# Kernel tuning notes

Measured on AMD Instinct MI355X. Metric: run time of the kernel, lower is better.

The kernel has to match this reference:

```python
import jax, jax.numpy as jnp
import numpy as np

HEADS = 8

def _conv(x, w, b, stride, pad):
    # x: [B,C,H,W], w: [O,I,kh,kw] (torch OIHW layout)
    y = jax.lax.conv_general_dilated(x, w, (stride, stride), ((pad, pad), (pad, pad)),
                                     dimension_numbers=('NCHW', 'OIHW', 'NCHW'))
    return y + b[None, :, None, None]

def _maxpool2x2(x):
    # returns pooled values and one-hot argmax per 2x2 window (torch first-max tie-break)
    b, c, H, W = x.shape
    win = x.reshape(b, c, H // 2, 2, W // 2, 2).transpose(0, 1, 2, 4, 3, 5).reshape(b, c, H // 2, W // 2, 4)
    am = jnp.argmax(win, axis=-1)
    oh = jax.nn.one_hot(am, 4, dtype=x.dtype)
    pooled = jnp.sum(win * oh, axis=-1)
    return pooled, oh

def _maxunpool2x2(y, oh):
    b, c, h2, w2 = y.shape
    out = y[..., None] * oh  # [b,c,h2,w2,4]
    out = out.reshape(b, c, h2, w2, 2, 2).transpose(0, 1, 2, 4, 3, 5).reshape(b, c, h2 * 2, w2 * 2)
    return out

def _mha2d(x, wq, wk, wv, wo):
    # x: [b,c,h,w]; wq/wk/wv/wo stored as [in,out] so y = x @ W
    b, c, h, w = x.shape
    hw = h * w
    dk = wq.shape[1]
    dh = dk // HEADS
    xt = x.reshape(b, c, hw).transpose(0, 2, 1)  # [b,hw,c]
    def split(y):  # torch: view(b,hw,dh,heads).permute(0,3,1,2)
        return y.reshape(b, hw, dh, HEADS).transpose(0, 3, 1, 2)  # [b,heads,hw,dh]
    q = split(xt @ wq)
    k = split(xt @ wk)
    v = split(xt @ wv)
    scale = jnp.sqrt(jnp.asarray(dh, x.dtype))
    attn = jax.nn.softmax(jnp.einsum('bhqd,bhkd->bhqk', q, k) / scale, axis=-1)
    o = jnp.einsum('bhqk,bhkd->bhqd', attn, v)
    o = o.transpose(0, 2, 3, 1).reshape(b, hw, dk)  # [b,hw,dh,heads] -> merge
    o = o @ wo
    return o.transpose(0, 2, 1).reshape(b, dk, h, w)

def setup_inputs() -> dict:
    key = jax.random.key(0)
    ks = jax.random.split(key, 10)
    B, C, H, W = 16, 256, 64, 64
    s = 0.05
    return {
        'x': jax.random.normal(ks[0], (B, C, H, W), jnp.float32),
        'conv_w': jax.random.normal(ks[1], (C, C, 3, 3), jnp.float32) * s,
        'conv_b': jax.random.normal(ks[2], (C,), jnp.float32) * s,
        'fr_w': jax.random.normal(ks[3], (C, C, 1, 1), jnp.float32) * s,
        'fr_b': jax.random.normal(ks[4], (C,), jnp.float32) * s,
        'wq': jax.random.normal(ks[5], (C, C), jnp.float32) * s,
        'wk': jax.random.normal(ks[6], (C, C), jnp.float32) * s,
        'wv': jax.random.normal(ks[7], (C, C), jnp.float32) * s,
        'wo': jax.random.normal(ks[8], (C, C), jnp.float32) * s,
        'gamma': jax.random.normal(ks[9], (1,), jnp.float32) * 0.1,
    }

def reference(x, conv_w, conv_b, fr_w, fr_b, wq, wk, wv, wo, gamma):
    _x = _conv(x, fr_w, fr_b, 1, 0)          # 1x1 feature reduction
    _x, oh = _maxpool2x2(_x)                 # MaxPool2d(2, return_indices=True)
    _x = _mha2d(_x, wq, wk, wv, wo)          # attention over pooled grid
    _x = _maxunpool2x2(_x, oh)               # MaxUnpool2d(2)
    return _x * jnp.tanh(gamma[0]) + _conv(x, conv_w, conv_b, 1, 1)
```

## Files before the change

### kernel.cpp

```cpp
#include <hip/hip_runtime.h>
#include <hip/hip_bf16.h>
#include <math.h>

#define B 16
#define C 256
#define H 64
#define W 64
#define H2 32
#define W2 32
#define HW2 1024
#define HEADS 8
#define DH 32

typedef unsigned short ushort_t;
using short8 = __attribute__((ext_vector_type(8))) short;
using u16x8  = __attribute__((ext_vector_type(8))) unsigned short;
using f32x4  = __attribute__((ext_vector_type(4))) float;

__device__ inline ushort_t f2bf(float f) {
    __hip_bfloat16 hb = __float2bfloat16(f);
    return *(ushort_t*)&hb;
}
__device__ inline float bf2f(ushort_t u) {
    return __uint_as_float(((unsigned)u) << 16);
}

__device__ __forceinline__ void cp16(const ushort_t* g, ushort_t* l) {
    __builtin_amdgcn_global_load_lds(
        (const __attribute__((address_space(1))) void*)g,
        (__attribute__((address_space(3))) void*)l, 16, 0, 0);
}

#define RSCALE 0.17677669529663687f

__global__ __launch_bounds__(256) void k_prep_wT(const float* __restrict__ cw,
                                                 ushort_t* __restrict__ wbfT) {
    int i = threadIdx.x, o = blockIdx.x;
    const float* src = cw + ((size_t)o * C + i) * 9;
#pragma unroll
    for (int kk = 0; kk < 9; kk++)
        wbfT[((size_t)kk * C + o) * C + i] = f2bf(src[kk]);
}

__global__ __launch_bounds__(256) void k_prep_wx(
    const float* __restrict__ wq, const float* __restrict__ wk,
    const float* __restrict__ wv, const float* __restrict__ wo,
    const float* __restrict__ frw, ushort_t* __restrict__ wqkvT,
    ushort_t* __restrict__ woT, ushort_t* __restrict__ wfr) {
    int op = blockIdx.x, mat = blockIdx.y, t = threadIdx.x;
    if (mat < 3) {
        const float* w = (mat == 0) ? wq : (mat == 1) ? wk : wv;
        int hh = op >> 5, d = op & 31, col = d * 8 + hh;
        wqkvT[(size_t)mat * 65536 + op * 256 + t] = f2bf(w[t * 256 + col]);
    } else if (mat == 3) {
        int hh = t >> 5, d = t & 31, ic = d * 8 + hh;
        woT[op * 256 + t] = f2bf(wo[ic * 256 + op]);
    } else {
        wfr[op * 256 + t] = f2bf(frw[op * 256 + t]);
    }
}

__global__ __launch_bounds__(256) void k_prep_xn(const float* __restrict__ x,
                                                 ushort_t* __restrict__ xn) {
    __shared__ ushort_t ldsT[64 * 258];
    int t = threadIdx.x;
    int hp = blockIdx.x, b = blockIdx.y;
    ushort_t* dst = xn + ((size_t)(b * 66 + hp)) * 66 * 256;

    if (hp == 0 || hp == 65) {
        u16x8 z = (u16x8){0, 0, 0, 0, 0, 0, 0, 0};
        for (int i = t; i < 2112; i += 256) *(u16x8*)(dst + i * 8) = z;
        return;
    }
    const float* xb = x + ((size_t)b * 256) * 4096 + (size_t)(hp - 1) * 64;
    {
        int cq = t >> 6, w = t & 63;
#pragma unroll 8
        for (int it = 0; it < 64; ++it) {
            int c = it * 4 + cq;
            float v = xb[(size_t)c * 4096 + w];
            ldsT[w * 258 + c] = f2bf(v);
        }
    }
    __syncthreads();
    {
        u16x8 z = (u16x8){0, 0, 0, 0, 0, 0, 0, 0};
        if (t < 32) *(u16x8*)(dst + t * 8) = z;
        else if (t < 64) *(u16x8*)(dst + 65 * 256 + (t - 32) * 8) = z;
    }
    {
        int half = t >> 7, cl = t & 127;
#pragma unroll 4
        for (int it = 0; it < 32; ++it) {
            int w = it * 2 + half;
            unsigned v = *(const unsigned*)&ldsT[w * 258 + cl * 2];
            *(unsigned*)(dst + (size_t)(w + 1) * 256 + cl * 2) = v;
        }
    }
}

__global__ __launch_bounds__(256) void k_conv1pool_mfma(
    const ushort_t* __restrict__ xn, const ushort_t* __restrict__ wfr,
    const float* __restrict__ frb, ushort_t* __restrict__ Pbf,
    unsigned char* __restrict__ idx) {
    __shared__ __align__(16) ushort_t sh[32768];
    ushort_t* Als = sh;
    ushort_t* Bls = sh + 8192;
    int t = threadIdx.x;
    int wg = blockIdx.x;
    int mt = (wg & 7) * 64 + (wg >> 3);
    int b = mt >> 5;
    int h0 = (mt * 2) & 63;

    int r = t >> 2, p = t & 3;
    int kswz = (p ^ ((r >> 1) & 3)) * 8;
    const ushort_t* aB0 = xn + ((size_t)((b * 66 + h0 + 1) * 66 + (r + 1))) * 256 + kswz;
    const ushort_t* aB1 = xn + ((size_t)((b * 66 + h0 + 2) * 66 + (r + 1))) * 256 + kswz;
    const ushort_t* bB = wfr + (size_t)r * 256 + kswz;

    f32x4 acc[4][8];
#pragma unroll
    for (int mf = 0; mf < 4; mf++)
#pragma unroll
        for (int nf = 0; nf < 8; nf++) acc[mf][nf] = (f32x4){0.f, 0.f, 0.f, 0.f};

    cp16(aB0, &Als[t * 8]);
    cp16(aB1, &Als[2048 + t * 8]);
    cp16(bB, &Bls[t * 8]);
    cp16(bB + 64 * 256, &Bls[2048 + t * 8]);
    cp16(bB + 128 * 256, &Bls[4096 + t * 8]);
    cp16(bB + 192 * 256, &Bls[6144 + t * 8]);
    __syncthreads();

    int l = t & 63, wid = t >> 6, wm = wid >> 1, wn = wid & 1;
    int arow = wm * 64 + (l & 15);
    int brow = wn * 128 + (l & 15);
    int pslot = ((l >> 4) ^ ((l >> 1) & 3)) * 8;

    for (int s = 0; s < 8; s++) {
        int cur = s & 1;
        if (s < 7) {
            int off = (s + 1) * 32;
            int nb = cur ^ 1;
            cp16(aB0 + off, &Als[nb * 4096 + t * 8]);
            cp16(aB1 + off, &Als[nb * 4096 + 2048 + t * 8]);
            cp16(bB + off, &Bls[nb * 8192 + t * 8]);
            cp16(bB + 64 * 256 + off, &Bls[nb * 8192 + 2048 + t * 8]);
            cp16(bB + 128 * 256 + off, &Bls[nb * 8192 + 4096 + t * 8]);
            cp16(bB + 192 * 256 + off, &Bls[nb * 8192 + 6144 + t * 8]);
        }
        short8 af[4], bf[8];
#pragma unroll
        for (int mf = 0; mf < 4; mf++)
            af[mf] = *(const short8*)&Als[cur * 4096 + (arow + mf * 16) * 32 + pslot];
#pragma unroll
        for (int nf = 0; nf < 8; nf++)
            bf[nf] = *(const short8*)&Bls[cur * 8192 + (brow + nf * 16) * 32 + pslot];
#pragma unroll
        for (int mf = 0; mf < 4; mf++)
#pragma unroll
            for (int nf = 0; nf < 8; nf++)
                acc[mf][nf] = __builtin_amdgcn_mfma_f32_16x16x32_bf16(
                    af[mf], bf[nf], acc[mf][nf], 0, 0, 0);
        __syncthreads();
    }

#pragma unroll
    for (int nf = 0; nf < 8; nf++) {
        int o = wn * 128 + nf * 16 + (l & 15);
        float bias = frb[o];
#pragma unroll
        for (int mf = 0; mf < 4; mf++) {
            int rbase = wm * 64 + mf * 16 + ((l >> 4) << 2);
            f32x4 a = acc[mf][nf];
#pragma unroll
            for (int jj = 0; jj < 4; jj++)
                sh[(rbase + jj) * 256 + o] = f2bf(a[jj] + bias);
        }
    }
    __syncthreads();

    {
        int h2 = mt & 31;
        size_t rowb = (size_t)(b << 10) + h2 * 32;
        int o0 = (t & 31) * 8;
#pragma unroll
        for (int pp = 0; pp < 4; pp++) {
            int w2 = pp * 8 + (t >> 5);
            u16x8 r0 = *(const u16x8*)&sh[(2 * w2) * 256 + o0];
            u16x8 r1 = *(const u16x8*)&sh[(2 * w2 + 1) * 256 + o0];
            u16x8 r2 = *(const u16x8*)&sh[(64 + 2 * w2) * 256 + o0];
            u16x8 r3 = *(const u16x8*)&sh[(64 + 2 * w2 + 1) * 256 + o0];
            u16x8 pv;
            unsigned amlo = 0, amhi = 0;
#pragma unroll
            for (int e = 0; e < 8; e++) {
                float v0 = bf2f(r0[e]), v1 = bf2f(r1[e]);
                float v2 = bf2f(r2[e]), v3 = bf2f(r3[e]);
                float m = v0;
                ushort_t raw = r0[e];
                unsigned am = 0;
                if (v1 > m) { m = v1; raw = r1[e]; am = 1; }
                if (v2 > m) { m = v2; raw = r2[e]; am = 2; }
                if (v3 > m) { m = v3; raw = r3[e]; am = 3; }
                pv[e] = raw;
                if (e < 4) amlo |= am << (8 * e);
                else       amhi |= am << (8 * (e - 4));
            }
            size_t po = (rowb + w2) * 256 + o0;
            *(u16x8*)(Pbf + po) = pv;
            *(uint2*)(idx + po) = make_uint2(amlo, amhi);
        }
    }
}

__global__ __launch_bounds__(256) void k_qkv_mfma(
    const ushort_t* __restrict__ A, const ushort_t* __restrict__ Bw,
    ushort_t* __restrict__ qb, ushort_t* __restrict__ kb,
    ushort_t* __restrict__ vtb) {
    __shared__ __align__(16) ushort_t Als[2][4096];
    __shared__ __align__(16) ushort_t Bls[2][4096];
    int t = threadIdx.x;
    int wg = blockIdx.x;
    int linear = (wg & 7) * 96 + (wg >> 3);
    int mt = linear / 6, nt = linear % 6;

    int r = t >> 2, p = t & 3;
    int kswz = (p ^ ((r >> 1) & 3)) * 8;
    const ushort_t* aB0 = A + ((size_t)(mt * 128 + r)) * 256 + kswz;
    const ushort_t* aB1 = aB0 + (size_t)64 * 256;
    const ushort_t* bB0 = Bw + ((size_t)(nt * 128 + r)) * 256 + kswz;
    const ushort_t* bB1 = bB0 + (size_t)64 * 256;

    f32x4 acc[4][4];
#pragma unroll
    for (int mf = 0; mf < 4; mf++)
#pragma unroll
        for (int nf = 0; nf < 4; nf++) acc[mf][nf] = (f32x4){0.f, 0.f, 0.f, 0.f};

    cp16(aB0, &Als[0][t * 8]);
    cp16(aB1, &Als[0][2048 + t * 8]);
    cp16(bB0, &Bls[0][t * 8]);
    cp16(bB1, &Bls[0][2048 + t * 8]);
    __syncthreads();

    int l = t & 63, wid = t >> 6, wm = wid >> 1, wn = wid & 1;
    int arow = wm * 64 + (l & 15);
    int brow = wn * 64 + (l & 15);
    int pslot = ((l >> 4) ^ ((l >> 1) & 3)) * 8;

    for (int s = 0; s < 8; s++) {
        int cur = s & 1;
        if (s < 7) {
            int off = (s + 1) * 32;
            int nb = cur ^ 1;
            cp16(aB0 + off, &Als[nb][t * 8]);
            cp16(aB1 + off, &Als[nb][2048 + t * 8]);
            cp16(bB0 + off, &Bls[nb][t * 8]);
            cp16(bB1 + off, &Bls[nb][2048 + t * 8]);
        }
        short8 af[4], bf[4];
#pragma unroll
        for (int mf = 0; mf < 4; mf++)
            af[mf] = *(const short8*)&Als[cur][(arow + mf * 16) * 32 + pslot];
#pragma unroll
        for (int nf = 0; nf < 4; nf++)
            bf[nf] = *(const short8*)&Bls[cur][(brow + nf * 16) * 32 + pslot];
#pragma unroll
        for (int mf = 0; mf < 4; mf++)
#pragma unroll
            for (int nf = 0; nf < 4; nf++)
                acc[mf][nf] = __builtin_amdgcn_mfma_f32_16x16x32_bf16(
                    af[mf], bf[nf], acc[mf][nf], 0, 0, 0);
        __syncthreads();
    }

    if (nt < 4) {
        ushort_t* dst = (nt < 2) ? qb : kb;
        float sc = (nt < 2) ? RSCALE : 1.0f;
        int ccb = (nt & 1) * 128 + wn * 64;
#pragma unroll
        for (int nf = 0; nf < 4; nf++) {
            int cc = ccb + nf * 16 + (l & 15);
#pragma unroll
            for (int mf = 0; mf < 4; mf++) {
                int m = mt * 128 + wm * 64 + mf * 16 + ((l >> 4) << 2);
                f32x4 a = acc[mf][nf];
#pragma unroll
                for (int jj = 0; jj < 4; jj++)
                    dst[(size_t)(m + jj) * 256 + cc] = f2bf(a[jj] * sc);
            }
        }
    } else {
#pragma unroll
        for (int nf = 0; nf < 4; nf++) {
            int cc = (nt & 1) * 128 + wn * 64 + nf * 16 + (l & 15);
#pragma unroll
            for (int mf = 0; mf < 4; mf++) {
                int m = mt * 128 + wm * 64 + mf * 16 + ((l >> 4) << 2);
                int b = m >> 10, n0 = m & 1023;
                f32x4 a = acc[mf][nf];
                unsigned u0 = ((unsigned)f2bf(a[1]) << 16) | f2bf(a[0]);
                unsigned u1 = ((unsigned)f2bf(a[3]) << 16) | f2bf(a[2]);
                *(uint2*)&vtb[((size_t)(b * 256 + cc)) * 1024 + n0] =
                    make_uint2(u0, u1);
            }
        }
    }
}

__global__ __launch_bounds__(256) void k_attn_mfma(
    const ushort_t* __restrict__ qb, const ushort_t* __restrict__ kb,
    const ushort_t* __restrict__ vtb, ushort_t* __restrict__ aoT) {
    __shared__ __align__(16) ushort_t Klds[2][2048];
    __shared__ __align__(16) ushort_t Vlds[2][2048];
    __shared__ __align__(16) ushort_t Plds[4][2304];
    __shared__ float rs_lds[128];

    int t = threadIdx.x;
    int bid = blockIdx.x;
    int swz = (bid & 7) * 128 + (bid >> 3);
    int bh = swz >> 3, qt = swz & 7;
    int b = bh >> 3, h = bh & 7;
    int w = t >> 6, l = t & 63, g = l >> 4, li = l & 15;

    size_t qrow = (size_t)(b * 1024 + qt * 128 + w * 32 + li);
    short8 qv0 = *(const short8*)(qb + qrow * 256 + h * 32 + g * 8);
    short8 qv1 = *(const short8*)(qb + (qrow + 16) * 256 + h * 32 + g * 8);

    int sr = t >> 2, sp = t & 3;
    const ushort_t* kg =
        kb + ((size_t)(b * 1024 + sr)) * 256 + h * 32 + ((sp ^ ((sr >> 1) & 3)) * 8);
    int vd = t >> 3, vs = t & 7;
    const ushort_t* vg =
        vtb + ((size_t)(b * 256 + h * 32 + vd)) * 1024 + ((vs ^ (vd & 7)) * 8);

    f32x4 oacc[2][2];
    f32x4 rsv[2];
#pragma unroll
    for (int qf = 0; qf < 2; qf++) {
        rsv[qf] = (f32x4){0.f, 0.f, 0.f, 0.f};
#pragma unroll
        for (int df = 0; df < 2; df++) oacc[qf][df] = (f32x4){0.f, 0.f, 0.f, 0.f};
    }

    cp16(kg, &Klds[0][t * 8]);
    cp16(vg, &Vlds[0][t * 8]);
    __syncthreads();

    ushort_t* Pw = &Plds[w][0];

    for (int c = 0; c < 16; c++) {
        int cur = c & 1;
        if (c < 15) {
            cp16(kg + (size_t)(c + 1) * 64 * 256, &Klds[cur ^ 1][t * 8]);
            cp16(vg + (c + 1) * 64, &Vlds[cur ^ 1][t * 8]);
        }
        short8 ak[4];
#pragma unroll
        for (int kf = 0; kf < 4; kf++)
            ak[kf] = *(const short8*)&Klds[cur][(16 * kf + li) * 32 +
                                               ((g ^ ((l >> 1) & 3)) * 8)];
#pragma unroll
        for (int qf = 0; qf < 2; qf++) {
            short8 qv = qf ? qv1 : qv0;
#pragma unroll
            for (int kf = 0; kf < 4; kf++) {
                f32x4 st = __builtin_amdgcn_mfma_f32_16x16x32_bf16(
                    ak[kf], qv, (f32x4){0.f, 0.f, 0.f, 0.f}, 0, 0, 0);
                float p0 = __expf(st[0]), p1 = __expf(st[1]);
                float p2 = __expf(st[2]), p3 = __expf(st[3]);
                rsv[qf][0] += p0; rsv[qf][1] += p1;
                rsv[qf][2] += p2; rsv[qf][3] += p3;
                unsigned u0, u1;
                asm("v_cvt_pk_bf16_f32 %0, %1, %2" : "=v"(u0) : "v"(p0), "v"(p1));
                asm("v_cvt_pk_bf16_f32 %0, %1, %2" : "=v"(u1) : "v"(p2), "v"(p3));
                *(uint2*)&Pw[(16 * qf + li) * 72 + 16 * kf + 4 * g] =
                    make_uint2(u0, u1);
            }
        }
#pragma unroll
        for (int win = 0; win < 2; win++) {
            short8 pa[2], bv[2];
#pragma unroll
            for (int qf = 0; qf < 2; qf++)
                pa[qf] = *(const short8*)&Pw[(16 * qf + li) * 72 + win * 32 + 8 * g];
#pragma unroll
            for (int df = 0; df < 2; df++)
                bv[df] = *(const short8*)&Vlds[cur][(16 * df + li) * 64 +
                                                    (((win * 4 + g) ^ (l & 7)) * 8)];
#pragma unroll
            for (int qf = 0; qf < 2; qf++)
#pragma unroll
                for (int df = 0; df < 2; df++)
                    oacc[qf][df] = __builtin_amdgcn_mfma_f32_16x16x32_bf16(
                        pa[qf], bv[df], oacc[qf][df], 0, 0, 0);
        }
        __syncthreads();
    }

#pragma unroll
    for (int qf = 0; qf < 2; qf++) {
        float rs = (rsv[qf][0] + rsv[qf][1]) + (rsv[qf][2] + rsv[qf][3]);
        rs += __shfl_xor(rs, 16);
        rs += __shfl_xor(rs, 32);
        if (l < 16) rs_lds[w * 32 + 16 * qf + li] = rs;
    }
    __syncthreads();

#pragma unroll
    for (int qf = 0; qf < 2; qf++) {
        float4 rs4 = *(const float4*)&rs_lds[w * 32 + 16 * qf + 4 * g];
        float inv[4] = {1.f / rs4.x, 1.f / rs4.y, 1.f / rs4.z, 1.f / rs4.w};
#pragma unroll
        for (int df = 0; df < 2; df++) {
            f32x4 a = oacc[qf][df];
#pragma unroll
            for (int r2 = 0; r2 < 4; r2++) {
                size_t row = (size_t)(b * 1024 + qt * 128 + w * 32 + 16 * qf +
                                      4 * g + r2);
                aoT[row * 256 + h * 32 + 16 * df + li] = f2bf(a[r2] * inv[r2]);
            }
        }
    }
}

__global__ __launch_bounds__(256) void k_oproj_mfma(
    const ushort_t* __restrict__ A, const ushort_t* __restrict__ Bw,
    float* __restrict__ y2) {
    __shared__ __align__(16) ushort_t Als[2][4096];
    __shared__ __align__(16) ushort_t Bls[2][4096];
    int t = threadIdx.x;
    int wg = blockIdx.x;
    int linear = (wg & 7) * 32 + (wg >> 3);
    int nt = linear & 1, mt = linear >> 1;

    int r = t >> 2, p = t & 3;
    int kswz = (p ^ ((r >> 1) & 3)) * 8;
    const ushort_t* aB0 = A + ((size_t)(mt * 128 + r)) * 256 + kswz;
    const ushort_t* aB1 = aB0 + (size_t)64 * 256;
    const ushort_t* bB0 = Bw + ((size_t)(nt * 128 + r)) * 256 + kswz;
    const ushort_t* bB1 = bB0 + (size_t)64 * 256;

    f32x4 acc[4][4];
#pragma unroll
    for (int mf = 0; mf < 4; mf++)
#pragma unroll
        for (int nf = 0; nf < 4; nf++) acc[mf][nf] = (f32x4){0.f, 0.f, 0.f, 0.f};

    cp16(aB0, &Als[0][t * 8]);
    cp16(aB1, &Als[0][2048 + t * 8]);
    cp16(bB0, &Bls[0][t * 8]);
    cp16(bB1, &Bls[0][2048 + t * 8]);
    __syncthreads();

    int l = t & 63, wid = t >> 6, wm = wid >> 1, wn = wid & 1;
    int arow = wm * 64 + (l & 15);
    int brow = wn * 64 + (l & 15);
    int pslot = ((l >> 4) ^ ((l >> 1) & 3)) * 8;

    for (int s = 0; s < 8; s++) {
        int cur = s & 1;
        if (s < 7) {
            int off = (s + 1) * 32;
            int nb = cur ^ 1;
            cp16(aB0 + off, &Als[nb][t * 8]);
            cp16(aB1 + off, &Als[nb][2048 + t * 8]);
            cp16(bB0 + off, &Bls[nb][t * 8]);
            cp16(bB1 + off, &Bls[nb][2048 + t * 8]);
        }
        short8 af[4], bf[4];
#pragma unroll
        for (int mf = 0; mf < 4; mf++)
            af[mf] = *(const short8*)&Als[cur][(arow + mf * 16) * 32 + pslot];
#pragma unroll
        for (int nf = 0; nf < 4; nf++)
            bf[nf] = *(const short8*)&Bls[cur][(brow + nf * 16) * 32 + pslot];
#pragma unroll
        for (int mf = 0; mf < 4; mf++)
#pragma unroll
            for (int nf = 0; nf < 4; nf++)
                acc[mf][nf] = __builtin_amdgcn_mfma_f32_16x16x32_bf16(
                    af[mf], bf[nf], acc[mf][nf], 0, 0, 0);
        __syncthreads();
    }

#pragma unroll
    for (int nf = 0; nf < 4; nf++) {
        int cc = nt * 128 + wn * 64 + nf * 16 + (l & 15);
#pragma unroll
        for (int mf = 0; mf < 4; mf++) {
            int m = mt * 128 + wm * 64 + mf * 16 + ((l >> 4) << 2);
            f32x4 a = acc[mf][nf];
#pragma unroll
            for (int jj = 0; jj < 4; jj++)
                y2[(size_t)(m + jj) * 256 + cc] = a[jj];
        }
    }
}

__global__ __launch_bounds__(512) void k_conv3_mfma(
    const ushort_t* __restrict__ xn, const ushort_t* __restrict__ wbfT,
    const float* __restrict__ cb, const float* __restrict__ y2,
    const unsigned char* __restrict__ idx, const float* __restrict__ gamma,
    float* __restrict__ out) {
    extern __shared__ __align__(16) ushort_t lds[];
    ushort_t* AL = lds;
    ushort_t* BL = lds + 32768;
    int t = threadIdx.x;
    int mt = blockIdx.x;

    int srow = t >> 3, sslot = t & 7;
    int kel = (sslot ^ (srow & 7)) * 8;
    const ushort_t* aP[2][2];
    const ushort_t* bP[2][2];
#pragma unroll
    for (int hf = 0; hf < 2; hf++)
#pragma unroll
        for (int j = 0; j < 2; j++) {
            int row = hf * 128 + j * 64 + srow;
            int m = mt * 256 + row;
            int b0 = m >> 12, h0 = (m >> 6) & 63, w0 = m & 63;
            aP[hf][j] = xn + ((size_t)((b0 * 66 + h0) * 66 + w0)) * 256 + kel;
            bP[hf][j] = wbfT + (size_t)row * 256 + kel;
        }

    auto offA = [](int kt) -> int {
        int khkw = kt >> 2, it = kt & 3;
        int kh = khkw / 3, kw = khkw - kh * 3;
        return (kh * 66 + kw) * 256 + it * 64;
    };
    auto offB = [](int kt) -> int {
        return (kt >> 2) * 65536 + (kt & 3) * 64;
    };
    auto STAGE_A = [&](int bb, int hf, int kt) {
        int o = offA(kt);
        ushort_t* d = AL + bb * 16384 + hf * 8192 + t * 8;
        cp16(aP[hf][0] + o, d);
        cp16(aP[hf][1] + o, d + 4096);
    };
    auto STAGE_B = [&](int bb, int hf, int kt) {
        int o = offB(kt);
        ushort_t* d = BL + bb * 16384 + hf * 8192 + t * 8;
        cp16(bP[hf][0] + o, d);
        cp16(bP[hf][1] + o, d + 4096);
    };

    f32x4 acc[8][4];
#pragma unroll
    for (int mf = 0; mf < 8; mf++)
#pragma unroll
        for (int nf = 0; nf < 4; nf++) acc[mf][nf] = (f32x4){0.f, 0.f, 0.f, 0.f};

    STAGE_A(0, 0, 0); STAGE_A(0, 1, 0); STAGE_B(0, 0, 0); STAGE_B(0, 1, 0);
    STAGE_B(1, 0, 1); STAGE_A(1, 0, 1);
    asm volatile("s_waitcnt vmcnt(4)" ::: "memory");
    __builtin_amdgcn_s_barrier();
    __builtin_amdgcn_sched_barrier(0);

    int l = t & 63, wid = t >> 6, wm = wid >> 2, wn = wid & 3;
    int lr = l & 15, g = l >> 4, l7 = l & 7;
    int abase = wm * 8192;
    int bbase = (wn >> 1) * 8192 + (wn & 1) * 4096;

    for (int kt = 0; kt < 36; kt++) {
        int bb = kt & 1;
        const ushort_t* Ab = AL + bb * 16384 + abase;
        const ushort_t* Bb = BL + bb * 16384 + bbase;
        short8 afA[4][2], afB[4][2], bf0[2][2], bf1[2][2];
#pragma unroll
        for (int mf = 0; mf < 4; mf++)
#pragma unroll
            for (int kk = 0; kk < 2; kk++)
                afA[mf][kk] = *(const short8*)
                    &Ab[(mf * 16 + lr) * 64 + (((kk * 4 + g) ^ l7) * 8)];
#pragma unroll
        for (int nf = 0; nf < 2; nf++)
#pragma unroll
            for (int kk = 0; kk < 2; kk++)
                bf0[nf][kk] = *(const short8*)
                    &Bb[(nf * 16 + lr) * 64 + (((kk * 4 + g) ^ l7) * 8)];
        if (kt < 35) STAGE_A(bb ^ 1, 1, kt + 1);
        asm volatile("" ::: "memory");
        __builtin_amdgcn_s_barrier();
        __builtin_amdgcn_sched_barrier(0);
        __builtin_amdgcn_s_setprio(1);
#pragma unroll
        for (int kk = 0; kk < 2; kk++)
#pragma unroll
            for (int mf = 0; mf < 4; mf++)
#pragma unroll
                for (int nf = 0; nf < 2; nf++)
                    acc[mf][nf] = __builtin_amdgcn_mfma_f32_16x16x32_bf16(
                        afA[mf][kk], bf0[nf][kk], acc[mf][nf], 0, 0, 0);
        __builtin_amdgcn_s_setprio(0);
        asm volatile("" ::: "memory");
        __builtin_amdgcn_s_barrier();
        __builtin_amdgcn_sched_barrier(0);
#pragma unroll
        for (int nf = 0; nf < 2; nf++)
#pragma unroll
            for (int kk = 0; kk < 2; kk++)
                bf1[nf][kk] = *(const short8*)
                    &Bb[((nf + 2) * 16 + lr) * 64 + (((kk * 4 + g) ^ l7) * 8)];
        if (kt < 35) STAGE_B(bb ^ 1, 1, kt + 1);
        asm volatile("" ::: "memory");
        __builtin_amdgcn_s_barrier();
        __builtin_amdgcn_sched_barrier(0);
        __builtin_amdgcn_s_setprio(1);
#pragma unroll
        for (int kk = 0; kk < 2; kk++)
#pragma unroll
            for (int mf = 0; mf < 4; mf++)
#pragma unroll
                for (int nf = 0; nf < 2; nf++)
                    acc[mf][nf + 2] = __builtin_amdgcn_mfma_f32_16x16x32_bf16(
                        afA[mf][kk], bf1[nf][kk], acc[mf][nf + 2], 0, 0, 0);
        __builtin_amdgcn_s_setprio(0);
        asm volatile("" ::: "memory");
        __builtin_amdgcn_s_barrier();
        __builtin_amdgcn_sched_barrier(0);
#pragma unroll
        for (int mf = 0; mf < 4; mf++)
#pragma unroll
            for (int kk = 0; kk < 2; kk++)
                afB[mf][kk] = *(const short8*)
                    &Ab[((mf + 4) * 16 + lr) * 64 + (((kk * 4 + g) ^ l7) * 8)];
        if (kt < 34) STAGE_B(bb, 0, kt + 2);
        asm volatile("" ::: "memory");
        __builtin_amdgcn_s_barrier();
        __builtin_amdgcn_sched_barrier(0);
        __builtin_amdgcn_s_setprio(1);
#pragma unroll
        for (int kk = 0; kk < 2; kk++)
#pragma unroll
            for (int mf = 0; mf < 4; mf++)
#pragma unroll
                for (int nf = 0; nf < 2; nf++)
                    acc[mf + 4][nf] = __builtin_amdgcn_mfma_f32_16x16x32_bf16(
                        afB[mf][kk], bf0[nf][kk], acc[mf + 4][nf], 0, 0, 0);
        __builtin_amdgcn_s_setprio(0);
        asm volatile("" ::: "memory");
        __builtin_amdgcn_s_barrier();
        __builtin_amdgcn_sched_barrier(0);
        if (kt < 34) {
            STAGE_A(bb, 0, kt + 2);
            asm volatile("s_waitcnt vmcnt(4)" ::: "memory");
        } else {
            asm volatile("s_waitcnt vmcnt(0)" ::: "memory");
        }
        __builtin_amdgcn_s_barrier();
        __builtin_amdgcn_sched_barrier(0);
        __builtin_amdgcn_s_setprio(1);
#pragma unroll
        for (int kk = 0; kk < 2; kk++)
#pragma unroll
            for (int mf = 0; mf < 4; mf++)
#pragma unroll
                for (int nf = 0; nf < 2; nf++)
                    acc[mf + 4][nf + 2] = __builtin_amdgcn_mfma_f32_16x16x32_bf16(
                        afB[mf][kk], bf1[nf][kk], acc[mf + 4][nf + 2], 0, 0, 0);
        __builtin_amdgcn_s_setprio(0);
        asm volatile("" ::: "memory");
        __builtin_amdgcn_s_barrier();
        __builtin_amdgcn_sched_barrier(0);
    }

    float tg = tanhf(gamma[0]);
    int mbase = mt * 256 + wm * 128 + (g << 2);
    int obase = wn * 64 + lr;
#pragma unroll
    for (int nf = 0; nf < 4; nf++) {
        int o = obase + nf * 16;
        float bias = cb[o];
#pragma unroll
        for (int mf = 0; mf < 8; mf++) {
            int m = mbase + mf * 16;
            int b = m >> 12, h = (m >> 6) & 63, w0 = m & 63;
            const unsigned char* idr = idx + ((size_t)(b << 10)) * 256;
            const float* y2r = y2 + ((size_t)(b << 10)) * 256;
            f32x4 a = acc[mf][nf];
            float v4[4];
#pragma unroll
            for (int jj = 0; jj < 4; jj++) {
                int wj = w0 + jj;
                int n2 = ((h >> 1) << 5) + (wj >> 1);
                int j2 = ((h & 1) << 1) + (wj & 1);
                float val = a[jj] + bias;
                if (idr[(size_t)n2 * 256 + o] == (unsigned char)j2)
                    val += tg * y2r[(size_t)n2 * 256 + o];
                v4[jj] = val;
            }
            *(float4*)(out + (((size_t)(b * C + o) * H + h) << 6) + w0) =
                make_float4(v4[0], v4[1], v4[2], v4[3]);
        }
    }
}

extern "C" void kernel_launch(void* const* d_in, const int* in_sizes, int n_in,
                              void* d_out, int out_size, void* d_ws, size_t ws_size,
                              hipStream_t stream) {
    const float* x      = (const float*)d_in[0];
    const float* conv_w = (const float*)d_in[1];
    const float* conv_b = (const float*)d_in[2];
    const float* fr_w   = (const float*)d_in[3];
    const float* fr_b   = (const float*)d_in[4];
    const float* wq     = (const float*)d_in[5];
    const float* wk     = (const float*)d_in[6];
    const float* wv     = (const float*)d_in[7];
    const float* wo     = (const float*)d_in[8];
    const float* gamma  = (const float*)d_in[9];
    float* out = (float*)d_out;
    char* ws = (char*)d_ws;

    ushort_t* wbfT  = (ushort_t*)(ws + 0);
    ushort_t* wfrbf = (ushort_t*)(ws + 1179648);
    ushort_t* wqkvT = (ushort_t*)(ws + 1310720);
    ushort_t* woT   = (ushort_t*)(ws + 1703936);
    ushort_t* xn    = (ushort_t*)(ws + 2097152);
    ushort_t* Pbf   = (ushort_t*)(ws + 37781504);
    unsigned char* idx = (unsigned char*)(ws + 46170112);
    ushort_t* qb    = (ushort_t*)(ws + 50364416);
    ushort_t* kb    = (ushort_t*)(ws + 58753024);
    ushort_t* vtb   = (ushort_t*)(ws + 67141632);
    ushort_t* aoT   = (ushort_t*)(ws + 75530240);
    float* y2       = (float*)(ws + 50364416);

    k_prep_wT<<<dim3(C), dim3(256), 0, stream>>>(conv_w, wbfT);
    k_prep_wx<<<dim3(256, 5), dim3(256), 0, stream>>>(wq, wk, wv, wo, fr_w,
                                                      wqkvT, woT, wfrbf);
    k_prep_xn<<<dim3(66, B), dim3(256), 0, stream>>>(x, xn);
    k_conv1pool_mfma<<<dim3(512), dim3(256), 0, stream>>>(xn, wfrbf, fr_b, Pbf, idx);
    k_qkv_mfma<<<dim3(768), dim3(256), 0, stream>>>(Pbf, wqkvT, qb, kb, vtb);
    k_attn_mfma<<<dim3(1024), dim3(256), 0, stream>>>(qb, kb, vtb, aoT);
    k_oproj_mfma<<<dim3(256), dim3(256), 0, stream>>>(aoT, woT, y2);
    (void)hipFuncSetAttribute(reinterpret_cast<const void*>(k_conv3_mfma),
                              hipFuncAttributeMaxDynamicSharedMemorySize, 131072);
    k_conv3_mfma<<<dim3(256), dim3(512), 131072, stream>>>(xn, wbfT, conv_b, y2, idx,
                                                           gamma, out);
    (void)in_sizes; (void)n_in; (void)out_size; (void)ws_size;
}
```

Baseline: 219.6 us.

## Reorder conv K-loop to channel-major taps and restructure ping-pong load schedule

Changes the K-tile iteration order of the 3x3 conv implicit GEMM so that the inner index walks the nine kernel taps before the channel chunk. It also reorganizes the four-phase MFMA/LDS/global-load schedule: A tiles for the next step are staged in the first two phases, both B halves are staged together later, and the number of barriers per iteration drops from eight to four. The aim is less synchronization overhead and better overlap of global loads with MFMA work. The trade-off is new LDS hazard timing, since the buffer-reuse ordering changed and the prologue now waits fully before issuing the second B stage.

```diff
diff --git a/kernel.cpp b/kernel.cpp
--- a/kernel.cpp
+++ b/kernel.cpp
@@ -526,12 +526,13 @@
         }
 
     auto offA = [](int kt) -> int {
-        int khkw = kt >> 2, it = kt & 3;
+        int it = kt / 9, khkw = kt - it * 9;
         int kh = khkw / 3, kw = khkw - kh * 3;
         return (kh * 66 + kw) * 256 + it * 64;
     };
     auto offB = [](int kt) -> int {
-        return (kt >> 2) * 65536 + (kt & 3) * 64;
+        int it = kt / 9, khkw = kt - it * 9;
+        return khkw * 65536 + it * 64;
     };
     auto STAGE_A = [&](int bb, int hf, int kt) {
         int o = offA(kt);
@@ -553,8 +554,8 @@
         for (int nf = 0; nf < 4; nf++) acc[mf][nf] = (f32x4){0.f, 0.f, 0.f, 0.f};
 
     STAGE_A(0, 0, 0); STAGE_A(0, 1, 0); STAGE_B(0, 0, 0); STAGE_B(0, 1, 0);
-    STAGE_B(1, 0, 1); STAGE_A(1, 0, 1);
-    asm volatile("s_waitcnt vmcnt(4)" ::: "memory");
+    asm volatile("s_waitcnt vmcnt(0)" ::: "memory");
+    STAGE_B(1, 0, 1); STAGE_B(1, 1, 1);
     __builtin_amdgcn_s_barrier();
     __builtin_amdgcn_sched_barrier(0);
 
@@ -564,9 +565,9 @@
     int bbase = (wn >> 1) * 8192 + (wn & 1) * 4096;
 
     for (int kt = 0; kt < 36; kt++) {
-        int bb = kt & 1;
-        const ushort_t* Ab = AL + bb * 16384 + abase;
-        const ushort_t* Bb = BL + bb * 16384 + bbase;
+        int cur = kt & 1, nxt = cur ^ 1;
+        const ushort_t* Ab = AL + cur * 16384 + abase;
+        const ushort_t* Bb = BL + cur * 16384 + bbase;
         short8 afA[4][2], afB[4][2], bf0[2][2], bf1[2][2];
 #pragma unroll
         for (int mf = 0; mf < 4; mf++)
@@ -578,10 +579,30 @@
         for (int nf = 0; nf < 2; nf++)
 #pragma unroll
             for (int kk = 0; kk < 2; kk++)
+                bf1[nf][kk] = *(const short8*)
+                    &Bb[((nf + 2) * 16 + lr) * 64 + (((kk * 4 + g) ^ l7) * 8)];
+        if (kt < 35) STAGE_A(nxt, 0, kt + 1);
+        __builtin_amdgcn_sched_barrier(0);
+        __builtin_amdgcn_s_barrier();
+        __builtin_amdgcn_sched_barrier(0);
+        __builtin_amdgcn_s_setprio(1);
+#pragma unroll
+        for (int kk = 0; kk < 2; kk++)
+#pragma unroll
+            for (int mf = 0; mf < 4; mf++)
+#pragma unroll
+                for (int nf = 0; nf < 2; nf++)
+                    acc[mf][nf + 2] = __builtin_amdgcn_mfma_f32_16x16x32_bf16(
+                        afA[mf][kk], bf1[nf][kk], acc[mf][nf + 2], 0, 0, 0);
+        __builtin_amdgcn_s_setprio(0);
+#pragma unroll
+        for (int nf = 0; nf < 2; nf++)
+#pragma unroll
+            for (int kk = 0; kk < 2; kk++)
                 bf0[nf][kk] = *(const short8*)
                     &Bb[(nf * 16 + lr) * 64 + (((kk * 4 + g) ^ l7) * 8)];
-        if (kt < 35) STAGE_A(bb ^ 1, 1, kt + 1);
-        asm volatile("" ::: "memory");
+        if (kt < 35) STAGE_A(nxt, 1, kt + 1);
+        __builtin_amdgcn_sched_barrier(0);
         __builtin_amdgcn_s_barrier();
         __builtin_amdgcn_sched_barrier(0);
         __builtin_amdgcn_s_setprio(1);
@@ -594,17 +615,13 @@
                     acc[mf][nf] = __builtin_amdgcn_mfma_f32_16x16x32_bf16(
                         afA[mf][kk], bf0[nf][kk], acc[mf][nf], 0, 0, 0);
         __builtin_amdgcn_s_setprio(0);
-        asm volatile("" ::: "memory");
-        __builtin_amdgcn_s_barrier();
+#pragma unroll
+        for (int mf = 0; mf < 4; mf++)
+#pragma unroll
+            for (int kk = 0; kk < 2; kk++)
+                afB[mf][kk] = *(const short8*)
+                    &Ab[((mf + 4) * 16 + lr) * 64 + (((kk * 4 + g) ^ l7) * 8)];
         __builtin_amdgcn_sched_barrier(0);
-#pragma unroll
-        for (int nf = 0; nf < 2; nf++)
-#pragma unroll
-            for (int kk = 0; kk < 2; kk++)
-                bf1[nf][kk] = *(const short8*)
-                    &Bb[((nf + 2) * 16 + lr) * 64 + (((kk * 4 + g) ^ l7) * 8)];
-        if (kt < 35) STAGE_B(bb ^ 1, 1, kt + 1);
-        asm volatile("" ::: "memory");
         __builtin_amdgcn_s_barrier();
         __builtin_amdgcn_sched_barrier(0);
         __builtin_amdgcn_s_setprio(1);
@@ -614,20 +631,17 @@
             for (int mf = 0; mf < 4; mf++)
 #pragma unroll
                 for (int nf = 0; nf < 2; nf++)
-                    acc[mf][nf + 2] = __builtin_amdgcn_mfma_f32_16x16x32_bf16(
-                        afA[mf][kk], bf1[nf][kk], acc[mf][nf + 2], 0, 0, 0);
+                    acc[mf + 4][nf + 2] = __builtin_amdgcn_mfma_f32_16x16x32_bf16(
+                        afB[mf][kk], bf1[nf][kk], acc[mf + 4][nf + 2], 0, 0, 0);
         __builtin_amdgcn_s_setprio(0);
-        asm volatile("" ::: "memory");
-        __builtin_amdgcn_s_barrier();
+        if (kt < 34) {
+            STAGE_B(cur, 0, kt + 2);
+            STAGE_B(cur, 1, kt + 2);
+            asm volatile("s_waitcnt vmcnt(4)" ::: "memory");
+        } else {
+            asm volatile("s_waitcnt vmcnt(0)" ::: "memory");
+        }
         __builtin_amdgcn_sched_barrier(0);
-#pragma unroll
-        for (int mf = 0; mf < 4; mf++)
-#pragma unroll
-            for (int kk = 0; kk < 2; kk++)
-                afB[mf][kk] = *(const short8*)
-                    &Ab[((mf + 4) * 16 + lr) * 64 + (((kk * 4 + g) ^ l7) * 8)];
-        if (kt < 34) STAGE_B(bb, 0, kt + 2);
-        asm volatile("" ::: "memory");
         __builtin_amdgcn_s_barrier();
         __builtin_amdgcn_sched_barrier(0);
         __builtin_amdgcn_s_setprio(1);
@@ -640,30 +654,6 @@
                     acc[mf + 4][nf] = __builtin_amdgcn_mfma_f32_16x16x32_bf16(
                         afB[mf][kk], bf0[nf][kk], acc[mf + 4][nf], 0, 0, 0);
         __builtin_amdgcn_s_setprio(0);
-        asm volatile("" ::: "memory");
-        __builtin_amdgcn_s_barrier();
-        __builtin_amdgcn_sched_barrier(0);
-        if (kt < 34) {
-            STAGE_A(bb, 0, kt + 2);
-            asm volatile("s_waitcnt vmcnt(4)" ::: "memory");
-        } else {
-            asm volatile("s_waitcnt vmcnt(0)" ::: "memory");
-        }
-        __builtin_amdgcn_s_barrier();
-        __builtin_amdgcn_sched_barrier(0);
-        __builtin_amdgcn_s_setprio(1);
-#pragma unroll
-        for (int kk = 0; kk < 2; kk++)
-#pragma unroll
-            for (int mf = 0; mf < 4; mf++)
-#pragma unroll
-                for (int nf = 0; nf < 2; nf++)
-                    acc[mf + 4][nf + 2] = __builtin_amdgcn_mfma_f32_16x16x32_bf16(
-                        afB[mf][kk], bf1[nf][kk], acc[mf + 4][nf + 2], 0, 0, 0);
-        __builtin_amdgcn_s_setprio(0);
-        asm volatile("" ::: "memory");
-        __builtin_amdgcn_s_barrier();
-        __builtin_amdgcn_sched_barrier(0);
     }
 
     float tg = tanhf(gamma[0]);
```

Result: faster. 213.1 us (-2.9%).
